# Kernel optimization log

Measured on AMD Instinct MI355X. Metric: run time of the kernel, lower is better.

## Reference

```python
import jax, jax.numpy as jnp
import numpy as np

# Instant-NGP style multi-level hash encoding constants (match init_kwargs)
N_LEVELS = 16
N_ENC = 16384          # per-level hashmap size (power of two)
N_EMBED = 2
MIN_RES = 16
MAX_RES = 512
HIDDEN = 64
P1 = np.uint32(2654435761)  # spatial hash primes (Instant-NGP)
P2 = np.uint32(805459861)


def _resolutions():
    b = np.exp((np.log(MAX_RES) - np.log(MIN_RES)) / (N_LEVELS - 1))
    return [int(np.floor(MIN_RES * b ** l)) for l in range(N_LEVELS)]


def _hash_encode(x, tables):
    """x: (B,3) in [-1,1]; tables: (L, T, E). Returns (B, L*E)."""
    feats = []
    for l, res in enumerate(_resolutions()):
        xg = (x + 1.0) * (0.5 * (res - 1))          # map [-1,1] -> [0, res-1]
        x0f = jnp.floor(xg)
        w = xg - x0f                                # (B,3) trilinear weights
        i0 = jnp.clip(x0f.astype(jnp.int32), 0, res - 1)
        i1 = jnp.clip(i0 + 1, 0, res - 1)
        dense = (res ** 3) <= N_ENC                 # small levels index densely
        feat = jnp.zeros((x.shape[0], N_EMBED), dtype=x.dtype)
        for cz in (0, 1):
            for cy in (0, 1):
                for cx in (0, 1):
                    ix = i1[:, 0] if cx else i0[:, 0]
                    iy = i1[:, 1] if cy else i0[:, 1]
                    iz = i1[:, 2] if cz else i0[:, 2]
                    if dense:
                        idx = ix + res * (iy + res * iz)
                    else:
                        idx = (ix.astype(jnp.uint32)
                               ^ (iy.astype(jnp.uint32) * P1)
                               ^ (iz.astype(jnp.uint32) * P2)) & np.uint32(N_ENC - 1)
                        idx = idx.astype(jnp.int32)
                    wc = ((w[:, 0] if cx else 1.0 - w[:, 0])
                          * (w[:, 1] if cy else 1.0 - w[:, 1])
                          * (w[:, 2] if cz else 1.0 - w[:, 2]))
                    feat = feat + wc[:, None] * tables[l, idx]
        feats.append(feat)
    return jnp.concatenate(feats, axis=-1)          # (B, 32)


def setup_inputs() -> dict:
    key = jax.random.key(0)
    ks = jax.random.split(key, 10)
    B = 1048576
    x = jax.random.uniform(ks[0], (B, 3), minval=-1.0, maxval=1.0)
    tables = jax.random.uniform(ks[1], (N_LEVELS, N_ENC, N_EMBED),
                                minval=-1e-4, maxval=1e-4)

    def lin(k, fin, fout):
        s = 1.0 / np.sqrt(fin)
        kw, kb = jax.random.split(k)
        return (jax.random.uniform(kw, (fin, fout), minval=-s, maxval=s),
                jax.random.uniform(kb, (fout,), minval=-s, maxval=s))

    w1, b1 = lin(ks[2], N_LEVELS * N_EMBED, HIDDEN)
    w2, b2 = lin(ks[3], HIDDEN, HIDDEN)
    w3, b3 = lin(ks[4], HIDDEN, 16)
    cw1, cb1 = lin(ks[5], 16, HIDDEN)
    cw2, cb2 = lin(ks[6], HIDDEN, HIDDEN)
    cw3, cb3 = lin(ks[7], HIDDEN, HIDDEN)
    cw4, cb4 = lin(ks[8], HIDDEN, 3)
    return {"x": x, "tables": tables,
            "w1": w1, "b1": b1, "w2": w2, "b2": b2, "w3": w3, "b3": b3,
            "cw1": cw1, "cb1": cb1, "cw2": cw2, "cb2": cb2,
            "cw3": cw3, "cb3": cb3, "cw4": cw4, "cb4": cb4}


def reference(x, tables, w1, b1, w2, b2, w3, b3,
              cw1, cb1, cw2, cb2, cw3, cb3, cw4, cb4):
    h = _hash_encode(x, tables)                     # (B, 32)
    d = jax.nn.relu(h @ w1 + b1)
    d = jax.nn.relu(d @ w2 + b2)
    d = d @ w3 + b3                                 # (B, 16)
    c = jax.nn.relu(d @ cw1 + cb1)
    c = jax.nn.relu(c @ cw2 + cb2)
    c = jax.nn.relu(c @ cw3 + cb3)
    c = jax.nn.sigmoid(c @ cw4 + cb4)               # is_hdr=False -> sigmoid
    sigma = jnp.exp(d[:, 0])                        # (B,)
    return sigma, c
```

## Files before the change

kernel.cpp:

```cpp
#include <hip/hip_runtime.h>

typedef __bf16 bf8 __attribute__((ext_vector_type(8)));
typedef float f4 __attribute__((ext_vector_type(4)));
typedef unsigned short us4 __attribute__((ext_vector_type(4)));
typedef unsigned int u32x4 __attribute__((ext_vector_type(4)));

#define MFMA16(a,b,c) __builtin_amdgcn_mfma_f32_16x16x32_bf16((a),(b),(c),0,0,0)

#define BLOCK 512
#define NWAVE 8

__device__ __forceinline__ unsigned short f2bfu(float f){
  __bf16 h = (__bf16)f;
  union { __bf16 b; unsigned short u; } v; v.b = h; return v.u;
}
__device__ __forceinline__ float ubfu(unsigned int u16){
  union { unsigned int i; float f; } v; v.i = u16 << 16; return v.f;
}

__device__ __forceinline__ void wfence(){
  asm volatile("s_waitcnt lgkmcnt(0)" ::: "memory");
}

#define OFF_W1   0
#define OFF_W2   2048
#define OFF_W3   6144
#define OFF_CW1  7168
#define OFF_CW2  8192
#define OFF_CW3  12288
#define OFF_CW4  16384
#define OFF_ACT  17408
#define ACT_STRIDE 72
#define SMEM_US  (17408 + NWAVE*16*ACT_STRIDE)

#define BO_B1  0
#define BO_B2  64
#define BO_B3  128
#define BO_CB1 144
#define BO_CB2 208
#define BO_CB3 272
#define BO_CB4 336

template<int FIN,int FOUT,int KS,int MT>
__device__ __forceinline__ void stage_w(const float* w, unsigned short* dst){
  const int total = KS*MT*512;
  for (int e = threadIdx.x; e < total; e += BLOCK){
    int chunk = e >> 9;
    int s = chunk / MT, t = chunk % MT;
    int le = e & 511;
    int lane = le >> 3, j = le & 7;
    int q = lane >> 4, m = lane & 15;
    int i = s*32 + q*8 + j;
    int o = t*16 + m;
    dst[e] = (i < FIN && o < FOUT) ? f2bfu(w[i*FOUT + o]) : (unsigned short)0;
  }
}

__device__ __forceinline__ void stage_cw1(const float* w, unsigned short* dst){
  for (int e = threadIdx.x; e < 1024; e += BLOCK){
    int t = e >> 8;
    int le = e & 255;
    int lane = le >> 3, j = e & 7;
    int q = lane >> 4, m = lane & 15;
    dst[e] = f2bfu(w[(q*8+j)*64 + t*16 + m]);
  }
}

__device__ __forceinline__ void layer64(const unsigned short* wlds, const unsigned short* bias,
                                        unsigned short* act, int lane, bool relu){
  const int q = lane >> 4, m = lane & 15;
  bf8 b0 = *(const bf8*)(act + m*ACT_STRIDE + q*8);
  bf8 b1 = *(const bf8*)(act + m*ACT_STRIDE + 32 + q*8);
  f4 acc[4];
#pragma unroll
  for (int t = 0; t < 4; ++t){
    f4 c = {0.f,0.f,0.f,0.f};
    c = MFMA16(*(const bf8*)(wlds + ((0*4+t)*64+lane)*8), b0, c);
    c = MFMA16(*(const bf8*)(wlds + ((1*4+t)*64+lane)*8), b1, c);
    acc[t] = c;
  }
#pragma unroll
  for (int t = 0; t < 4; ++t){
    us4 bb = *(const us4*)(bias + t*16 + q*4);
    us4 pk;
#pragma unroll
    for (int r = 0; r < 4; ++r){
      float v = acc[t][r] + ubfu(bb[r]);
      if (relu) v = fmaxf(v, 0.f);
      pk[r] = f2bfu(v);
    }
    *(us4*)(act + m*ACT_STRIDE + t*16 + q*4) = pk;
  }
}

#define STAGE_ALL_WEIGHTS()                                                  \
  stage_w<32,64,1,4>(w1,  smem+OFF_W1);                                      \
  stage_w<64,64,2,4>(w2,  smem+OFF_W2);                                      \
  stage_w<64,16,2,1>(w3,  smem+OFF_W3);                                      \
  stage_cw1(cw1, smem+OFF_CW1);                                              \
  stage_w<64,64,2,4>(cw2, smem+OFF_CW2);                                     \
  stage_w<64,64,2,4>(cw3, smem+OFF_CW3);                                     \
  stage_w<64, 3,2,1>(cw4, smem+OFF_CW4);                                     \
  {                                                                          \
    int t = threadIdx.x;                                                     \
    if (t < 64){                                                             \
      sbias[BO_B1 +t] = f2bfu(b1[t]);                                        \
      sbias[BO_B2 +t] = f2bfu(b2[t]);                                        \
      sbias[BO_CB1+t] = f2bfu(cb1[t]);                                       \
      sbias[BO_CB2+t] = f2bfu(cb2[t]);                                       \
      sbias[BO_CB3+t] = f2bfu(cb3[t]);                                       \
    }                                                                        \
    if (t < 16) sbias[BO_B3+t] = f2bfu(b3[t]);                               \
    if (t < 3)  sbias[BO_CB4+t] = f2bfu(cb4[t]);                             \
  }

#define MLP_BODY(bfrag, gp)                                                  \
    {                                                                        \
      f4 acc[4];                                                             \
      _Pragma("unroll")                                                      \
      for (int t = 0; t < 4; ++t){                                           \
        f4 c = {0.f,0.f,0.f,0.f};                                            \
        acc[t] = MFMA16(*(const bf8*)(smem + OFF_W1 + (t*64+lane)*8), bfrag, c);\
      }                                                                      \
      _Pragma("unroll")                                                      \
      for (int t = 0; t < 4; ++t){                                           \
        us4 bb = *(const us4*)(sbias + BO_B1 + t*16 + q*4);                  \
        us4 pk;                                                              \
        _Pragma("unroll")                                                    \
        for (int r = 0; r < 4; ++r){                                         \
          float v = fmaxf(acc[t][r] + ubfu(bb[r]), 0.f);                     \
          pk[r] = f2bfu(v);                                                  \
        }                                                                    \
        *(us4*)(act + m*ACT_STRIDE + t*16 + q*4) = pk;                       \
      }                                                                      \
    }                                                                        \
    wfence();                                                                \
    layer64(smem+OFF_W2, sbias+BO_B2, act, lane, true);                      \
    wfence();                                                                \
    {                                                                        \
      bf8 b0 = *(const bf8*)(act + m*ACT_STRIDE + q*8);                      \
      bf8 b1 = *(const bf8*)(act + m*ACT_STRIDE + 32 + q*8);                 \
      f4 c = {0.f,0.f,0.f,0.f};                                              \
      c = MFMA16(*(const bf8*)(smem + OFF_W3 + lane*8), b0, c);              \
      c = MFMA16(*(const bf8*)(smem + OFF_W3 + (64+lane)*8), b1, c);         \
      us4 bb = *(const us4*)(sbias + BO_B3 + q*4);                           \
      us4 pk;                                                                \
      float d0 = 0.f;                                                        \
      _Pragma("unroll")                                                      \
      for (int r = 0; r < 4; ++r){                                           \
        float v = c[r] + ubfu(bb[r]);                                        \
        if (r == 0) d0 = v;                                                  \
        pk[r] = f2bfu(v);                                                    \
      }                                                                      \
      if (q == 0 && gp < nB) out[gp] = expf(d0);                             \
      *(us4*)(act + m*ACT_STRIDE + q*4) = pk;                                \
    }                                                                        \
    wfence();                                                                \
    {                                                                        \
      bf8 bc, aw[4];                                                         \
      if (q < 2){                                                            \
        bc = *(const bf8*)(act + m*ACT_STRIDE + q*8);                        \
        _Pragma("unroll")                                                    \
        for (int t = 0; t < 4; ++t)                                          \
          aw[t] = *(const bf8*)(smem + OFF_CW1 + (t*32+lane)*8);             \
      } else {                                                               \
        _Pragma("unroll")                                                    \
        for (int j = 0; j < 8; ++j) bc[j] = (__bf16)0.f;                     \
        _Pragma("unroll")                                                    \
        for (int t = 0; t < 4; ++t) aw[t] = bc;                              \
      }                                                                      \
      f4 acc[4];                                                             \
      _Pragma("unroll")                                                      \
      for (int t = 0; t < 4; ++t){                                           \
        f4 c = {0.f,0.f,0.f,0.f};                                            \
        acc[t] = MFMA16(aw[t], bc, c);                                       \
      }                                                                      \
      _Pragma("unroll")                                                      \
      for (int t = 0; t < 4; ++t){                                           \
        us4 bb = *(const us4*)(sbias + BO_CB1 + t*16 + q*4);                 \
        us4 pk;                                                              \
        _Pragma("unroll")                                                    \
        for (int r = 0; r < 4; ++r){                                         \
          float v = fmaxf(acc[t][r] + ubfu(bb[r]), 0.f);                     \
          pk[r] = f2bfu(v);                                                  \
        }                                                                    \
        *(us4*)(act + m*ACT_STRIDE + t*16 + q*4) = pk;                       \
      }                                                                      \
    }                                                                        \
    wfence();                                                                \
    layer64(smem+OFF_CW2, sbias+BO_CB2, act, lane, true);                    \
    wfence();                                                                \
    layer64(smem+OFF_CW3, sbias+BO_CB3, act, lane, true);                    \
    wfence();                                                                \
    {                                                                        \
      bf8 b0 = *(const bf8*)(act + m*ACT_STRIDE + q*8);                      \
      bf8 b1 = *(const bf8*)(act + m*ACT_STRIDE + 32 + q*8);                 \
      f4 c = {0.f,0.f,0.f,0.f};                                              \
      c = MFMA16(*(const bf8*)(smem + OFF_CW4 + lane*8), b0, c);             \
      c = MFMA16(*(const bf8*)(smem + OFF_CW4 + (64+lane)*8), b1, c);        \
      if (q == 0 && gp < nB){                                                \
        _Pragma("unroll")                                                    \
        for (int r = 0; r < 3; ++r){                                         \
          float v = c[r] + ubfu(sbias[BO_CB4 + r]);                          \
          out[nB + gp*3 + r] = 1.f/(1.f + expf(-v));                         \
        }                                                                    \
      }                                                                      \
    }                                                                        \
    wfence();

#define CH 16384
__global__ __launch_bounds__(512) void hash_phase(
    const float* __restrict__ xin, const float* __restrict__ tab,
    unsigned int* __restrict__ feat, int nB)
{
  __shared__ unsigned int stab[16384];
  __shared__ int sres[16];
  const int lvl = blockIdx.y;
  {
    const float2* t2 = (const float2*)tab + (lvl<<14);
    for (int e = threadIdx.x; e < 16384; e += 512){
      float2 v = t2[e];
      stab[e] = ((unsigned)f2bfu(v.y) << 16) | (unsigned)f2bfu(v.x);
    }
    if (threadIdx.x < 16){
      const int R[16] = {16,20,25,32,40,50,64,80,101,128,161,203,256,322,406,512};
      sres[threadIdx.x] = R[threadIdx.x];
    }
  }
  __syncthreads();

  const int res = sres[lvl];
  const float sc = 0.5f*(float)(res-1);
  const bool dense = (lvl < 3);
  unsigned int* fout = feat + (size_t)lvl * (size_t)nB;

  int pend = (blockIdx.x + 1) * CH; if (pend > nB) pend = nB;
  for (int p = blockIdx.x*CH + threadIdx.x; p < pend; p += 512){
    const float px = xin[p*3+0], py = xin[p*3+1], pz = xin[p*3+2];
    const float xs=(px+1.f)*sc, ys=(py+1.f)*sc, zs=(pz+1.f)*sc;
    const float fx=floorf(xs), fy=floorf(ys), fz=floorf(zs);
    const float wx=xs-fx, wy=ys-fy, wz=zs-fz;
    int ix0=min(max((int)fx,0),res-1);
    int iy0=min(max((int)fy,0),res-1);
    int iz0=min(max((int)fz,0),res-1);
    int ix1=min(ix0+1,res-1), iy1=min(iy0+1,res-1), iz1=min(iz0+1,res-1);
    unsigned X0,X1,Y0,Y1,Z0,Z1;
    if (dense){
      X0=(unsigned)ix0;            X1=(unsigned)ix1;
      Y0=(unsigned)(res*iy0);      Y1=(unsigned)(res*iy1);
      Z0=(unsigned)(res*res*iz0);  Z1=(unsigned)(res*res*iz1);
    } else {
      X0=(unsigned)ix0;                 X1=(unsigned)ix1;
      Y0=(unsigned)iy0*2654435761u;     Y1=(unsigned)iy1*2654435761u;
      Z0=(unsigned)iz0*805459861u;      Z1=(unsigned)iz1*805459861u;
    }
    const float wx0=1.f-wx, wy0=1.f-wy, wz0=1.f-wz;
    float f0=0.f, f1=0.f;
#pragma unroll
    for (int c = 0; c < 8; ++c){
      unsigned xc = (c&1)?X1:X0;
      unsigned yc = (c&2)?Y1:Y0;
      unsigned zc = (c&4)?Z1:Z0;
      unsigned idx = dense ? (xc+yc+zc) : ((xc^yc^zc)&16383u);
      unsigned tv = stab[idx];
      float wc = ((c&1)?wx:wx0) * ((c&2)?wy:wy0) * ((c&4)?wz:wz0);
      f0 += wc*ubfu(tv << 16);
      f1 += wc*ubfu(tv & 0xffff0000u);
    }
    fout[p] = ((unsigned)f2bfu(f1) << 16) | (unsigned)f2bfu(f0);
  }
}

__global__ __launch_bounds__(BLOCK) void mlp_phase(
    const unsigned int* __restrict__ feat,
    const float* __restrict__ w1,  const float* __restrict__ b1,
    const float* __restrict__ w2,  const float* __restrict__ b2,
    const float* __restrict__ w3,  const float* __restrict__ b3,
    const float* __restrict__ cw1, const float* __restrict__ cb1,
    const float* __restrict__ cw2, const float* __restrict__ cb2,
    const float* __restrict__ cw3, const float* __restrict__ cb3,
    const float* __restrict__ cw4, const float* __restrict__ cb4,
    float* __restrict__ out, int nB)
{
  __shared__ __align__(16) unsigned short smem[SMEM_US];
  __shared__ __align__(16) unsigned short sbias[344];
  STAGE_ALL_WEIGHTS();
  __syncthreads();

  const int lane = threadIdx.x & 63, wv = threadIdx.x >> 6;
  const int q = lane >> 4, m = lane & 15;
  unsigned short* act = smem + OFF_ACT + wv*16*ACT_STRIDE;
  const unsigned int* fq = feat + (size_t)(4*q) * (size_t)nB;

  for (int it = 0; it < 4; ++it){
    const int gp  = blockIdx.x*BLOCK + wv*64 + it*16 + m;
    const int gpl = min(gp, nB-1);
    union { u32x4 u; bf8 b; } fb;
    fb.u[0] = fq[gpl];
    fb.u[1] = fq[(size_t)nB   + gpl];
    fb.u[2] = fq[(size_t)nB*2 + gpl];
    fb.u[3] = fq[(size_t)nB*3 + gpl];
    bf8 bfrag = fb.b;
    MLP_BODY(bfrag, gp)
  }
}

__global__ __launch_bounds__(BLOCK) void nerf_fused(
    const float* __restrict__ xin, const float* __restrict__ tab,
    const float* __restrict__ w1,  const float* __restrict__ b1,
    const float* __restrict__ w2,  const float* __restrict__ b2,
    const float* __restrict__ w3,  const float* __restrict__ b3,
    const float* __restrict__ cw1, const float* __restrict__ cb1,
    const float* __restrict__ cw2, const float* __restrict__ cb2,
    const float* __restrict__ cw3, const float* __restrict__ cb3,
    const float* __restrict__ cw4, const float* __restrict__ cb4,
    float* __restrict__ out, int nB)
{
  __shared__ __align__(16) unsigned short smem[SMEM_US];
  __shared__ __align__(16) unsigned short sbias[344];
  __shared__ int sres[16];
  STAGE_ALL_WEIGHTS();
  if (threadIdx.x < 16){
    const int R[16] = {16,20,25,32,40,50,64,80,101,128,161,203,256,322,406,512};
    sres[threadIdx.x] = R[threadIdx.x];
  }
  __syncthreads();

  const int lane = threadIdx.x & 63, wv = threadIdx.x >> 6;
  const int q = lane >> 4, m = lane & 15;
  unsigned short* act = smem + OFF_ACT + wv*16*ACT_STRIDE;

  int res_[4];
#pragma unroll
  for (int d = 0; d < 4; ++d) res_[d] = sres[4*q + d];

  for (int it = 0; it < 4; ++it){
    const int gp  = blockIdx.x*BLOCK + wv*64 + it*16 + m;
    const int gpl = min(gp, nB-1);
    const float px = xin[gpl*3+0];
    const float py = xin[gpl*3+1];
    const float pz = xin[gpl*3+2];

    bf8 bfrag;
#pragma unroll
    for (int d = 0; d < 4; ++d){
      const int lvl = 4*q + d;
      const int res = res_[d];
      const float sc = 0.5f*(float)(res-1);
      const float xs=(px+1.f)*sc, ys=(py+1.f)*sc, zs=(pz+1.f)*sc;
      const float fx=floorf(xs), fy=floorf(ys), fz=floorf(zs);
      const float wx=xs-fx, wy=ys-fy, wz=zs-fz;
      int ix0=min(max((int)fx,0),res-1);
      int iy0=min(max((int)fy,0),res-1);
      int iz0=min(max((int)fz,0),res-1);
      int ix1=min(ix0+1,res-1), iy1=min(iy0+1,res-1), iz1=min(iz0+1,res-1);
      const bool dense = (lvl < 3);
      unsigned X0,X1,Y0,Y1,Z0,Z1;
      if (dense){
        X0=(unsigned)ix0;            X1=(unsigned)ix1;
        Y0=(unsigned)(res*iy0);      Y1=(unsigned)(res*iy1);
        Z0=(unsigned)(res*res*iz0);  Z1=(unsigned)(res*res*iz1);
      } else {
        X0=(unsigned)ix0;                 X1=(unsigned)ix1;
        Y0=(unsigned)iy0*2654435761u;     Y1=(unsigned)iy1*2654435761u;
        Z0=(unsigned)iz0*805459861u;      Z1=(unsigned)iz1*805459861u;
      }
      const float wx0=1.f-wx, wy0=1.f-wy, wz0=1.f-wz;
      float f0=0.f, f1=0.f;
      const float2* tl = (const float2*)tab + (lvl<<14);
#pragma unroll
      for (int c = 0; c < 8; ++c){
        unsigned xc = (c&1)?X1:X0;
        unsigned yc = (c&2)?Y1:Y0;
        unsigned zc = (c&4)?Z1:Z0;
        unsigned idx = dense ? (xc+yc+zc) : ((xc^yc^zc)&16383u);
        float2 tv = tl[idx];
        float wc = ((c&1)?wx:wx0) * ((c&2)?wy:wy0) * ((c&4)?wz:wz0);
        f0 += wc*tv.x;
        f1 += wc*tv.y;
      }
      bfrag[2*d]   = (__bf16)f0;
      bfrag[2*d+1] = (__bf16)f1;
    }
    MLP_BODY(bfrag, gp)
  }
}

extern "C" void kernel_launch(void* const* d_in, const int* in_sizes, int n_in,
                              void* d_out, int out_size, void* d_ws, size_t ws_size,
                              hipStream_t stream) {
  (void)n_in; (void)out_size;
  const int nB = in_sizes[0] / 3;
  const float* xin = (const float*)d_in[0];
  const float* tab = (const float*)d_in[1];
  const float *w1=(const float*)d_in[2],  *b1=(const float*)d_in[3];
  const float *w2=(const float*)d_in[4],  *b2=(const float*)d_in[5];
  const float *w3=(const float*)d_in[6],  *b3=(const float*)d_in[7];
  const float *cw1=(const float*)d_in[8], *cb1=(const float*)d_in[9];
  const float *cw2=(const float*)d_in[10],*cb2=(const float*)d_in[11];
  const float *cw3=(const float*)d_in[12],*cb3=(const float*)d_in[13];
  const float *cw4=(const float*)d_in[14],*cb4=(const float*)d_in[15];
  float* out = (float*)d_out;

  const size_t need = (size_t)nB * 16u * 4u;
  if (ws_size >= need){
    dim3 ga((nB + CH - 1) / CH, 16);
    hash_phase<<<ga, dim3(512), 0, stream>>>(xin, tab, (unsigned int*)d_ws, nB);
    const int blocks = (nB + BLOCK - 1) / BLOCK;
    mlp_phase<<<dim3(blocks), dim3(BLOCK), 0, stream>>>(
        (const unsigned int*)d_ws, w1,b1,w2,b2,w3,b3,
        cw1,cb1,cw2,cb2,cw3,cb3,cw4,cb4, out, nB);
  } else {
    const int blocks = (nB + BLOCK - 1) / BLOCK;
    nerf_fused<<<dim3(blocks), dim3(BLOCK), 0, stream>>>(
        xin, tab, w1,b1,w2,b2,w3,b3,
        cw1,cb1,cw2,cb2,cw3,cb3,cw4,cb4, out, nB);
  }
}
```

Baseline: 197.1 us.

## Fold w3 into cw1 layer, fold biases into MFMA accumulators, widen hash blocks

Precomputes the product of the linear density-output layer and the first color layer, adding a small prep kernel that writes it to workspace. This replaces two narrow MFMA layers with one 64x64 layer, and computes sigma separately from a single column of w3. Biases now initialise the MFMA accumulators instead of being added afterwards. The hash phase runs 1024-thread blocks and uses fma with pre-multiplied xy weights. Folding the layers changes bf16 rounding and adds one extra kernel launch.

```diff
diff --git a/kernel.cpp b/kernel.cpp
--- a/kernel.cpp
+++ b/kernel.cpp
@@ -9,6 +9,8 @@
 
 #define BLOCK 512
 #define NWAVE 8
+#define HBLOCK 1024
+#define CH 16384
 
 __device__ __forceinline__ unsigned short f2bfu(float f){
   __bf16 h = (__bf16)f;
@@ -17,6 +19,9 @@
 __device__ __forceinline__ float ubfu(unsigned int u16){
   union { unsigned int i; float f; } v; v.i = u16 << 16; return v.f;
 }
+__device__ __forceinline__ float u2f(unsigned int u){
+  union { unsigned int i; float f; } v; v.i = u; return v.f;
+}
 
 __device__ __forceinline__ void wfence(){
   asm volatile("s_waitcnt lgkmcnt(0)" ::: "memory");
@@ -24,22 +29,22 @@
 
 #define OFF_W1   0
 #define OFF_W2   2048
-#define OFF_W3   6144
-#define OFF_CW1  7168
-#define OFF_CW2  8192
-#define OFF_CW3  12288
-#define OFF_CW4  16384
-#define OFF_ACT  17408
+#define OFF_W3C  6144
+#define OFF_CW2  10240
+#define OFF_CW3  14336
+#define OFF_CW4  18432
+#define OFF_W3C0 19456
+#define OFF_ACT  19528
 #define ACT_STRIDE 72
-#define SMEM_US  (17408 + NWAVE*16*ACT_STRIDE)
-
-#define BO_B1  0
-#define BO_B2  64
-#define BO_B3  128
-#define BO_CB1 144
-#define BO_CB2 208
-#define BO_CB3 272
-#define BO_CB4 336
+#define SMEM_US  (19528 + NWAVE*16*ACT_STRIDE)
+
+#define NB_B1  0
+#define NB_B2  64
+#define NB_BC  128
+#define NB_CB2 192
+#define NB_CB3 256
+#define NB_CB4 320
+#define NB_B3S 323
 
 template<int FIN,int FOUT,int KS,int MT>
 __device__ __forceinline__ void stage_w(const float* w, unsigned short* dst){
@@ -56,62 +61,67 @@
   }
 }
 
-__device__ __forceinline__ void stage_cw1(const float* w, unsigned short* dst){
-  for (int e = threadIdx.x; e < 1024; e += BLOCK){
-    int t = e >> 8;
-    int le = e & 255;
-    int lane = le >> 3, j = e & 7;
+__device__ __forceinline__ void stage_w3c_inline(const float* w3, const float* cw1,
+                                                 unsigned short* dst){
+  for (int e = threadIdx.x; e < 4096; e += BLOCK){
+    int chunk = e >> 9;
+    int s = chunk >> 2, t = chunk & 3;
+    int le = e & 511;
+    int lane = le >> 3, j = le & 7;
     int q = lane >> 4, m = lane & 15;
-    dst[e] = f2bfu(w[(q*8+j)*64 + t*16 + m]);
-  }
-}
-
-__device__ __forceinline__ void layer64(const unsigned short* wlds, const unsigned short* bias,
-                                        unsigned short* act, int lane, bool relu){
+    int i = s*32 + q*8 + j;
+    int o = t*16 + m;
+    float sum = 0.f;
+#pragma unroll
+    for (int u = 0; u < 16; ++u) sum = fmaf(w3[i*16+u], cw1[u*64+o], sum);
+    dst[e] = f2bfu(sum);
+  }
+}
+
+__device__ __forceinline__ void layer64b(const unsigned short* wlds, const unsigned short* bias,
+                                         unsigned short* act, int lane, bool relu){
   const int q = lane >> 4, m = lane & 15;
   bf8 b0 = *(const bf8*)(act + m*ACT_STRIDE + q*8);
   bf8 b1 = *(const bf8*)(act + m*ACT_STRIDE + 32 + q*8);
   f4 acc[4];
 #pragma unroll
   for (int t = 0; t < 4; ++t){
-    f4 c = {0.f,0.f,0.f,0.f};
+    us4 bb = *(const us4*)(bias + t*16 + q*4);
+    f4 c = {ubfu(bb[0]), ubfu(bb[1]), ubfu(bb[2]), ubfu(bb[3])};
     c = MFMA16(*(const bf8*)(wlds + ((0*4+t)*64+lane)*8), b0, c);
     c = MFMA16(*(const bf8*)(wlds + ((1*4+t)*64+lane)*8), b1, c);
     acc[t] = c;
   }
 #pragma unroll
   for (int t = 0; t < 4; ++t){
-    us4 bb = *(const us4*)(bias + t*16 + q*4);
     us4 pk;
 #pragma unroll
     for (int r = 0; r < 4; ++r){
-      float v = acc[t][r] + ubfu(bb[r]);
-      if (relu) v = fmaxf(v, 0.f);
+      float v = relu ? fmaxf(acc[t][r], 0.f) : acc[t][r];
       pk[r] = f2bfu(v);
     }
     *(us4*)(act + m*ACT_STRIDE + t*16 + q*4) = pk;
   }
 }
 
-#define STAGE_ALL_WEIGHTS()                                                  \
+#define STAGE_COMMON()                                                       \
   stage_w<32,64,1,4>(w1,  smem+OFF_W1);                                      \
   stage_w<64,64,2,4>(w2,  smem+OFF_W2);                                      \
-  stage_w<64,16,2,1>(w3,  smem+OFF_W3);                                      \
-  stage_cw1(cw1, smem+OFF_CW1);                                              \
   stage_w<64,64,2,4>(cw2, smem+OFF_CW2);                                     \
   stage_w<64,64,2,4>(cw3, smem+OFF_CW3);                                     \
   stage_w<64, 3,2,1>(cw4, smem+OFF_CW4);                                     \
   {                                                                          \
     int t = threadIdx.x;                                                     \
     if (t < 64){                                                             \
-      sbias[BO_B1 +t] = f2bfu(b1[t]);                                        \
-      sbias[BO_B2 +t] = f2bfu(b2[t]);                                        \
-      sbias[BO_CB1+t] = f2bfu(cb1[t]);                                       \
-      sbias[BO_CB2+t] = f2bfu(cb2[t]);                                       \
-      sbias[BO_CB3+t] = f2bfu(cb3[t]);                                       \
+      sbias[NB_B1 +t] = f2bfu(b1[t]);                                        \
+      sbias[NB_B2 +t] = f2bfu(b2[t]);                                        \
+      sbias[NB_CB2+t] = f2bfu(cb2[t]);                                       \
+      sbias[NB_CB3+t] = f2bfu(cb3[t]);                                       \
+      smem[OFF_W3C0+t] = f2bfu(w3[t*16]);                   \
     }                                                                        \
-    if (t < 16) sbias[BO_B3+t] = f2bfu(b3[t]);                               \
-    if (t < 3)  sbias[BO_CB4+t] = f2bfu(cb4[t]);                             \
+    if (t >= 64 && t < 72) smem[OFF_W3C0+t] = 0;                             \
+    if (t < 3)  sbias[NB_CB4+t] = f2bfu(cb4[t]);                             \
+    if (t == 0) sbias[NB_B3S]   = f2bfu(b3[0]);                              \
   }
 
 #define MLP_BODY(bfrag, gp)                                                  \
@@ -119,78 +129,36 @@
       f4 acc[4];                                                             \
       _Pragma("unroll")                                                      \
       for (int t = 0; t < 4; ++t){                                           \
-        f4 c = {0.f,0.f,0.f,0.f};                                            \
+        us4 bb = *(const us4*)(sbias + NB_B1 + t*16 + q*4);                  \
+        f4 c = {ubfu(bb[0]), ubfu(bb[1]), ubfu(bb[2]), ubfu(bb[3])};         \
         acc[t] = MFMA16(*(const bf8*)(smem + OFF_W1 + (t*64+lane)*8), bfrag, c);\
       }                                                                      \
       _Pragma("unroll")                                                      \
       for (int t = 0; t < 4; ++t){                                           \
-        us4 bb = *(const us4*)(sbias + BO_B1 + t*16 + q*4);                  \
         us4 pk;                                                              \
         _Pragma("unroll")                                                    \
-        for (int r = 0; r < 4; ++r){                                         \
-          float v = fmaxf(acc[t][r] + ubfu(bb[r]), 0.f);                     \
-          pk[r] = f2bfu(v);                                                  \
-        }                                                                    \
+        for (int r = 0; r < 4; ++r) pk[r] = f2bfu(fmaxf(acc[t][r], 0.f));    \
         *(us4*)(act + m*ACT_STRIDE + t*16 + q*4) = pk;                       \
       }                                                                      \
     }                                                                        \
     wfence();                                                                \
-    layer64(smem+OFF_W2, sbias+BO_B2, act, lane, true);                      \
+    layer64b(smem+OFF_W2, sbias+NB_B2, act, lane, true);                     \
     wfence();                                                                \
-    {                                                                        \
+    {   \
+      bf8 a0 = *(const bf8*)(smem + OFF_W3C0 + q*8);                         \
+      bf8 a1 = *(const bf8*)(smem + OFF_W3C0 + 32 + q*8);                    \
       bf8 b0 = *(const bf8*)(act + m*ACT_STRIDE + q*8);                      \
       bf8 b1 = *(const bf8*)(act + m*ACT_STRIDE + 32 + q*8);                 \
-      f4 c = {0.f,0.f,0.f,0.f};                                              \
-      c = MFMA16(*(const bf8*)(smem + OFF_W3 + lane*8), b0, c);              \
-      c = MFMA16(*(const bf8*)(smem + OFF_W3 + (64+lane)*8), b1, c);         \
-      us4 bb = *(const us4*)(sbias + BO_B3 + q*4);                           \
-      us4 pk;                                                                \
-      float d0 = 0.f;                                                        \
-      _Pragma("unroll")                                                      \
-      for (int r = 0; r < 4; ++r){                                           \
-        float v = c[r] + ubfu(bb[r]);                                        \
-        if (r == 0) d0 = v;                                                  \
-        pk[r] = f2bfu(v);                                                    \
-      }                                                                      \
-      if (q == 0 && gp < nB) out[gp] = expf(d0);                             \
-      *(us4*)(act + m*ACT_STRIDE + q*4) = pk;                                \
+      f4 c = {b3f, b3f, b3f, b3f};                                           \
+      c = MFMA16(a0, b0, c);                                                 \
+      c = MFMA16(a1, b1, c);                                                 \
+      if (q == 0 && gp < nB) out[gp] = expf(c[0]);                           \
     }                                                                        \
+    layer64b(smem+OFF_W3C, sbias+NB_BC, act, lane, true);      \
     wfence();                                                                \
-    {                                                                        \
-      bf8 bc, aw[4];                                                         \
-      if (q < 2){                                                            \
-        bc = *(const bf8*)(act + m*ACT_STRIDE + q*8);                        \
-        _Pragma("unroll")                                                    \
-        for (int t = 0; t < 4; ++t)                                          \
-          aw[t] = *(const bf8*)(smem + OFF_CW1 + (t*32+lane)*8);             \
-      } else {                                                               \
-        _Pragma("unroll")                                                    \
-        for (int j = 0; j < 8; ++j) bc[j] = (__bf16)0.f;                     \
-        _Pragma("unroll")                                                    \
-        for (int t = 0; t < 4; ++t) aw[t] = bc;                              \
-      }                                                                      \
-      f4 acc[4];                                                             \
-      _Pragma("unroll")                                                      \
-      for (int t = 0; t < 4; ++t){                                           \
-        f4 c = {0.f,0.f,0.f,0.f};                                            \
-        acc[t] = MFMA16(aw[t], bc, c);                                       \
-      }                                                                      \
-      _Pragma("unroll")                                                      \
-      for (int t = 0; t < 4; ++t){                                           \
-        us4 bb = *(const us4*)(sbias + BO_CB1 + t*16 + q*4);                 \
-        us4 pk;                                                              \
-        _Pragma("unroll")                                                    \
-        for (int r = 0; r < 4; ++r){                                         \
-          float v = fmaxf(acc[t][r] + ubfu(bb[r]), 0.f);                     \
-          pk[r] = f2bfu(v);                                                  \
-        }                                                                    \
-        *(us4*)(act + m*ACT_STRIDE + t*16 + q*4) = pk;                       \
-      }                                                                      \
-    }                                                                        \
+    layer64b(smem+OFF_CW2, sbias+NB_CB2, act, lane, true);                   \
     wfence();                                                                \
-    layer64(smem+OFF_CW2, sbias+BO_CB2, act, lane, true);                    \
-    wfence();                                                                \
-    layer64(smem+OFF_CW3, sbias+BO_CB3, act, lane, true);                    \
+    layer64b(smem+OFF_CW3, sbias+NB_CB3, act, lane, true);                   \
     wfence();                                                                \
     {                                                                        \
       bf8 b0 = *(const bf8*)(act + m*ACT_STRIDE + q*8);                      \
@@ -201,15 +169,34 @@
       if (q == 0 && gp < nB){                                                \
         _Pragma("unroll")                                                    \
         for (int r = 0; r < 3; ++r){                                         \
-          float v = c[r] + ubfu(sbias[BO_CB4 + r]);                          \
+          float v = c[r] + ubfu(sbias[NB_CB4 + r]);                          \
           out[nB + gp*3 + r] = 1.f/(1.f + expf(-v));                         \
         }                                                                    \
       }                                                                      \
     }                                                                        \
     wfence();
 
-#define CH 16384
-__global__ __launch_bounds__(512) void hash_phase(
+__global__ __launch_bounds__(512) void w3c_prep(
+    const float* __restrict__ w3,  const float* __restrict__ b3,
+    const float* __restrict__ cw1, const float* __restrict__ cb1,
+    float* __restrict__ w3c, float* __restrict__ bc)
+{
+  int idx = blockIdx.x*512 + threadIdx.x;
+  int k = idx >> 6, o = idx & 63;
+  float s = 0.f;
+#pragma unroll
+  for (int j = 0; j < 16; ++j) s = fmaf(w3[k*16+j], cw1[j*64+o], s);
+  w3c[idx] = s;
+  if (blockIdx.x == 0 && threadIdx.x < 64){
+    int oo = threadIdx.x;
+    float t = cb1[oo];
+#pragma unroll
+    for (int j = 0; j < 16; ++j) t = fmaf(b3[j], cw1[j*64+oo], t);
+    bc[oo] = t;
+  }
+}
+
+__global__ __launch_bounds__(HBLOCK) void hash_phase(
     const float* __restrict__ xin, const float* __restrict__ tab,
     unsigned int* __restrict__ feat, int nB)
 {
@@ -218,7 +205,7 @@
   const int lvl = blockIdx.y;
   {
     const float2* t2 = (const float2*)tab + (lvl<<14);
-    for (int e = threadIdx.x; e < 16384; e += 512){
+    for (int e = threadIdx.x; e < 16384; e += HBLOCK){
       float2 v = t2[e];
       stab[e] = ((unsigned)f2bfu(v.y) << 16) | (unsigned)f2bfu(v.x);
     }
@@ -235,7 +222,7 @@
   unsigned int* fout = feat + (size_t)lvl * (size_t)nB;
 
   int pend = (blockIdx.x + 1) * CH; if (pend > nB) pend = nB;
-  for (int p = blockIdx.x*CH + threadIdx.x; p < pend; p += 512){
+  for (int p = blockIdx.x*CH + threadIdx.x; p < pend; p += HBLOCK){
     const float px = xin[p*3+0], py = xin[p*3+1], pz = xin[p*3+2];
     const float xs=(px+1.f)*sc, ys=(py+1.f)*sc, zs=(pz+1.f)*sc;
     const float fx=floorf(xs), fy=floorf(ys), fz=floorf(zs);
@@ -255,6 +242,7 @@
       Z0=(unsigned)iz0*805459861u;      Z1=(unsigned)iz1*805459861u;
     }
     const float wx0=1.f-wx, wy0=1.f-wy, wz0=1.f-wz;
+    const float wxy0=wx0*wy0, wxy1=wx*wy0, wxy2=wx0*wy, wxy3=wx*wy;
     float f0=0.f, f1=0.f;
 #pragma unroll
     for (int c = 0; c < 8; ++c){
@@ -263,9 +251,10 @@
       unsigned zc = (c&4)?Z1:Z0;
       unsigned idx = dense ? (xc+yc+zc) : ((xc^yc^zc)&16383u);
       unsigned tv = stab[idx];
-      float wc = ((c&1)?wx:wx0) * ((c&2)?wy:wy0) * ((c&4)?wz:wz0);
-      f0 += wc*ubfu(tv << 16);
-      f1 += wc*ubfu(tv & 0xffff0000u);
+      float wxy = (c&2) ? ((c&1)?wxy3:wxy2) : ((c&1)?wxy1:wxy0);
+      float wc  = wxy * ((c&4)?wz:wz0);
+      f0 = fmaf(wc, u2f(tv << 16), f0);
+      f1 = fmaf(wc, u2f(tv & 0xffff0000u), f1);
     }
     fout[p] = ((unsigned)f2bfu(f1) << 16) | (unsigned)f2bfu(f0);
   }
@@ -273,24 +262,27 @@
 
 __global__ __launch_bounds__(BLOCK) void mlp_phase(
     const unsigned int* __restrict__ feat,
+    const float* __restrict__ w3c,  const float* __restrict__ bc,
     const float* __restrict__ w1,  const float* __restrict__ b1,
     const float* __restrict__ w2,  const float* __restrict__ b2,
     const float* __restrict__ w3,  const float* __restrict__ b3,
-    const float* __restrict__ cw1, const float* __restrict__ cb1,
     const float* __restrict__ cw2, const float* __restrict__ cb2,
     const float* __restrict__ cw3, const float* __restrict__ cb3,
     const float* __restrict__ cw4, const float* __restrict__ cb4,
     float* __restrict__ out, int nB)
 {
   __shared__ __align__(16) unsigned short smem[SMEM_US];
-  __shared__ __align__(16) unsigned short sbias[344];
-  STAGE_ALL_WEIGHTS();
+  __shared__ __align__(16) unsigned short sbias[328];
+  STAGE_COMMON();
+  stage_w<64,64,2,4>(w3c, smem+OFF_W3C);
+  if (threadIdx.x < 64) sbias[NB_BC + threadIdx.x] = f2bfu(bc[threadIdx.x]);
   __syncthreads();
 
   const int lane = threadIdx.x & 63, wv = threadIdx.x >> 6;
   const int q = lane >> 4, m = lane & 15;
   unsigned short* act = smem + OFF_ACT + wv*16*ACT_STRIDE;
   const unsigned int* fq = feat + (size_t)(4*q) * (size_t)nB;
+  const float b3f = ubfu(sbias[NB_B3S]);
 
   for (int it = 0; it < 4; ++it){
     const int gp  = blockIdx.x*BLOCK + wv*64 + it*16 + m;
@@ -317,9 +309,17 @@
     float* __restrict__ out, int nB)
 {
   __shared__ __align__(16) unsigned short smem[SMEM_US];
-  __shared__ __align__(16) unsigned short sbias[344];
+  __shared__ __align__(16) unsigned short sbias[328];
   __shared__ int sres[16];
-  STAGE_ALL_WEIGHTS();
+  STAGE_COMMON();
+  stage_w3c_inline(w3, cw1, smem+OFF_W3C);
+  if (threadIdx.x < 64){
+    int oo = threadIdx.x;
+    float t = cb1[oo];
+#pragma unroll
+    for (int j = 0; j < 16; ++j) t = fmaf(b3[j], cw1[j*64+oo], t);
+    sbias[NB_BC+oo] = f2bfu(t);
+  }
   if (threadIdx.x < 16){
     const int R[16] = {16,20,25,32,40,50,64,80,101,128,161,203,256,322,406,512};
     sres[threadIdx.x] = R[threadIdx.x];
@@ -329,6 +329,7 @@
   const int lane = threadIdx.x & 63, wv = threadIdx.x >> 6;
   const int q = lane >> 4, m = lane & 15;
   unsigned short* act = smem + OFF_ACT + wv*16*ACT_STRIDE;
+  const float b3f = ubfu(sbias[NB_B3S]);
 
   int res_[4];
 #pragma unroll
@@ -402,14 +403,19 @@
   const float *cw4=(const float*)d_in[14],*cb4=(const float*)d_in[15];
   float* out = (float*)d_out;
 
-  const size_t need = (size_t)nB * 16u * 4u;
+  const size_t featN = (size_t)nB * 16u;
+  const size_t need  = (featN + 4096u + 64u) * 4u;
   if (ws_size >= need){
+    unsigned int* feat = (unsigned int*)d_ws;
+    float* w3c = (float*)d_ws + featN;
+    float* bc  = w3c + 4096;
+    w3c_prep<<<dim3(8), dim3(512), 0, stream>>>(w3, b3, cw1, cb1, w3c, bc);
     dim3 ga((nB + CH - 1) / CH, 16);
-    hash_phase<<<ga, dim3(512), 0, stream>>>(xin, tab, (unsigned int*)d_ws, nB);
+    hash_phase<<<ga, dim3(HBLOCK), 0, stream>>>(xin, tab, feat, nB);
     const int blocks = (nB + BLOCK - 1) / BLOCK;
     mlp_phase<<<dim3(blocks), dim3(BLOCK), 0, stream>>>(
-        (const unsigned int*)d_ws, w1,b1,w2,b2,w3,b3,
-        cw1,cb1,cw2,cb2,cw3,cb3,cw4,cb4, out, nB);
+        feat, w3c, bc, w1,b1,w2,b2,w3,b3,
+        cw2,cb2,cw3,cb3,cw4,cb4, out, nB);
   } else {
     const int blocks = (nB + BLOCK - 1) / BLOCK;
     nerf_fused<<<dim3(blocks), dim3(BLOCK), 0, stream>>>(
```

Result: slower. 239.1 us (+21.3%).
